# Kernel optimization log

Hardware: AMD Instinct MI355X
Metric: run time of the kernel (lower is better)

The kernel has to match this reference:

```python
import jax, jax.numpy as jnp
import numpy as np

N = 50000      # nodes
E = 1600000    # edges (avg degree 32)
IN, H, OUT, ED = 16, 128, 64, 16


def setup_inputs() -> dict:
    key = jax.random.key(0)
    ks = jax.random.split(key, 24)

    def w(k, shape):
        return jax.random.normal(k, shape, jnp.float32) / np.float32(np.sqrt(shape[0]))

    inp = {
        "x": jax.random.normal(ks[0], (N, IN), jnp.float32),
        "edge_attr": jax.random.normal(ks[1], (E, ED), jnp.float32),
        "edge_src": jax.random.randint(ks[2], (E,), 0, N, jnp.int32),
        "edge_dst": jax.random.randint(ks[3], (E,), 0, N, jnp.int32),
    }
    dims = [(IN, H, H), (H, H, H), (H, H, OUT)]
    i = 4
    for l, (din, dh, dout) in enumerate(dims):
        inp[f"we{l}"] = w(ks[i], (ED, din)); inp[f"be{l}"] = jnp.zeros((din,), jnp.float32)
        inp[f"w1{l}"] = w(ks[i + 1], (din, dh)); inp[f"b1{l}"] = jnp.zeros((dh,), jnp.float32)
        inp[f"w2{l}"] = w(ks[i + 2], (dh, dout)); inp[f"b2{l}"] = jnp.zeros((dout,), jnp.float32)
        i += 3
    inp["rw1"] = w(ks[i], (OUT, H)); inp["rb1"] = jnp.zeros((H,), jnp.float32)
    inp["rw2"] = w(ks[i + 1], (H, IN)); inp["rb2"] = jnp.zeros((IN,), jnp.float32)
    return inp


def reference(x, edge_attr, edge_src, edge_dst,
              we0, be0, w10, b10, w20, b20,
              we1, be1, w11, b11, w21, b21,
              we2, be2, w12, b12, w22, b22,
              rw1, rb1, rw2, rb2):
    layers = [(we0, be0, w10, b10, w20, b20),
              (we1, be1, w11, b11, w21, b21),
              (we2, be2, w12, b12, w22, b22)]
    n = x.shape[0]

    def phi(h):
        # GIN with edge features (GINE): h_i = MLP(h_i + sum_j relu(h_j + W_e e_ij))
        for idx, (we, be, w1, b1, w2, b2) in enumerate(layers):
            e = edge_attr @ we + be                                  # [E, d_in]
            msg = jax.nn.relu(h[edge_src] + e)                       # [E, d_in]
            agg = jax.ops.segment_sum(msg, edge_dst, num_segments=n)  # [N, d_in]
            h = jax.nn.relu((h + agg) @ w1 + b1) @ w2 + b2           # conv MLP
            if idx < len(layers) - 1:
                h = jax.nn.relu(h)
        return h

    out = phi(x) + phi(-x)                       # sign invariance, [N, OUT]
    out = jax.nn.relu(out @ rw1 + rb1) @ rw2 + rb2  # rho readout, [N, IN]
    return out
```

## Files before the change

### kernel.cpp

```cpp
#include <hip/hip_runtime.h>

constexpr int DHID = 128;

typedef __attribute__((ext_vector_type(8))) short bf16x8v;
typedef __attribute__((ext_vector_type(4))) float f32x4v;

__device__ __forceinline__ float b2f(unsigned short u) {
    union { unsigned int i; float f; } v;
    v.i = ((unsigned int)u) << 16;
    return v.f;
}
__device__ __forceinline__ unsigned short f2b(float f) {
    union { float f; unsigned int i; } v;
    v.f = f;
    unsigned int x = v.i;
    return (unsigned short)((x + 0x7fff + ((x >> 16) & 1)) >> 16);
}
__device__ __forceinline__ unsigned int pack2(float a, float b) {
    return (unsigned int)f2b(a) | ((unsigned int)f2b(b) << 16);
}
__device__ __forceinline__ float bres(float w) { return w - b2f(f2b(w)); }
__device__ __forceinline__ void dot2b(float& acc, unsigned int a, unsigned int b) {
    asm("v_dot2_f32_bf16 %0, %1, %2, %0" : "+v"(acc) : "v"(a), "v"(b));
}

__global__ __launch_bounds__(256)
void init_h0(const float* __restrict__ x, float* __restrict__ H0,
             unsigned short* __restrict__ H0B, int n) {
    int i = blockIdx.x * 256 + threadIdx.x;
    if (i < n * 16) {
        int r = i >> 4, c = i & 15;
        float v = x[i];
        H0[(size_t)(2 * r) * 16 + c] = v;
        H0[(size_t)(2 * r + 1) * 16 + c] = -v;
        H0B[(size_t)(2 * r) * 16 + c] = f2b(v);
        H0B[(size_t)(2 * r + 1) * 16 + c] = f2b(-v);
    }
}

__global__ __launch_bounds__(256)
void sum_signs(const float* __restrict__ H3, float* __restrict__ S, int n) {
    int i = blockIdx.x * 256 + threadIdx.x;
    if (i < n * 64) {
        int r = i >> 6;
        S[i] = H3[i + (size_t)r * 64] + H3[i + (size_t)r * 64 + 64];
    }
}

__global__ __launch_bounds__(256)
void csr_count(const int* __restrict__ DST, int* __restrict__ deg, int E_) {
    int e = blockIdx.x * 256 + threadIdx.x;
    if (e < E_) atomicAdd(&deg[DST[e]], 1);
}

__global__ __launch_bounds__(256)
void scan1(const int* __restrict__ deg, int* __restrict__ off,
           int* __restrict__ bsum, int n) {
    __shared__ int s[256];
    int tid = threadIdx.x;
    int i = blockIdx.x * 256 + tid;
    int v = (i < n) ? deg[i] : 0;
    s[tid] = v;
    __syncthreads();
    for (int d = 1; d < 256; d <<= 1) {
        int t = (tid >= d) ? s[tid - d] : 0;
        __syncthreads();
        if (tid >= d) s[tid] += t;
        __syncthreads();
    }
    if (i < n) off[i] = s[tid] - v;
    if (tid == 255) bsum[blockIdx.x] = s[255];
}

__global__ __launch_bounds__(256)
void scan2(int* __restrict__ bsum, int nb) {
    __shared__ int s[256];
    int tid = threadIdx.x;
    int v = (tid < nb) ? bsum[tid] : 0;
    s[tid] = v;
    __syncthreads();
    for (int d = 1; d < 256; d <<= 1) {
        int t = (tid >= d) ? s[tid - d] : 0;
        __syncthreads();
        if (tid >= d) s[tid] += t;
        __syncthreads();
    }
    if (tid < nb) bsum[tid] = s[tid] - v;
}

__global__ __launch_bounds__(256)
void scan3(int* __restrict__ off, int* __restrict__ pos,
           const int* __restrict__ bsum, const int* __restrict__ deg, int n) {
    int i = blockIdx.x * 256 + threadIdx.x;
    if (i < n) {
        int o = off[i] + bsum[blockIdx.x];
        off[i] = o;
        pos[i] = o;
        if (i == n - 1) off[n] = o + deg[i];
    }
}

__global__ __launch_bounds__(256)
void csr_fill(const int* __restrict__ SRC, const int* __restrict__ DST,
              const float* __restrict__ EA, int* __restrict__ pos,
              int* __restrict__ csrsrc, uint4* __restrict__ EABS, int E_) {
    int e = blockIdx.x * 256 + threadIdx.x;
    if (e < E_) {
        int d = DST[e];
        int j = atomicAdd(&pos[d], 1);
        csrsrc[j] = SRC[e];
        const float4* ea4 = (const float4*)(EA + (size_t)e * 16);
        float4 q0 = ea4[0], q1 = ea4[1], q2 = ea4[2], q3 = ea4[3];
        uint4 o0, o1;
        o0.x = pack2(q0.x, q0.y); o0.y = pack2(q0.z, q0.w);
        o0.z = pack2(q1.x, q1.y); o0.w = pack2(q1.z, q1.w);
        o1.x = pack2(q2.x, q2.y); o1.y = pack2(q2.z, q2.w);
        o1.z = pack2(q3.x, q3.y); o1.w = pack2(q3.z, q3.w);
        EABS[(size_t)2 * j] = o0;
        EABS[(size_t)2 * j + 1] = o1;
    }
}

__global__ __launch_bounds__(256)
void agg_gather128(const int* __restrict__ CSRS, const int* __restrict__ OFF,
                   const unsigned short* __restrict__ EABS,
                   const float* __restrict__ WE, const float* __restrict__ BE,
                   const unsigned short* __restrict__ HB,
                   float* __restrict__ AGG, int n) {
    __shared__ float esm_all[4][16][132];
    const int tid = threadIdx.x;
    const int wv = tid >> 6;
    const int lane = tid & 63;
    const int node = blockIdx.x * 4 + wv;
    if (node >= n) return;
    float (*esm)[132] = esm_all[wv];

    const int col = lane & 15;
    const int grp = lane >> 4;
    const int klo = (grp & 1) * 8;

    bf16x8v bfrag[8];
#pragma unroll
    for (int cb = 0; cb < 8; ++cb) {
        bf16x8v b;
#pragma unroll
        for (int i = 0; i < 8; ++i) {
            float w = WE[(klo + i) * 128 + cb * 16 + col];
            unsigned short hi = f2b(w);
            unsigned short lo = f2b(bres(w));
            b[i] = (short)(grp >= 2 ? lo : hi);
        }
        bfrag[cb] = b;
    }
    float bias[8];
#pragma unroll
    for (int cb = 0; cb < 8; ++cb) bias[cb] = BE[cb * 16 + col];

    const int o = lane & 31;
    const int s = o >> 4;
    const int co = (o & 15) * 8;
    const int ep = lane >> 5;

    float acc[8];
#pragma unroll
    for (int i = 0; i < 8; ++i) acc[i] = 0.f;

    const int j0 = OFF[node], j1 = OFF[node + 1];
    const char* ebase = (const char*)EABS;

    for (int base = j0; base < j1; base += 16) {
        const int rem = j1 - base;
        uint4 a4 = *(const uint4*)(ebase + ((size_t)(base + col) << 5) +
                                   ((grp & 1) << 4));
        bf16x8v afrag = __builtin_bit_cast(bf16x8v, a4);
#pragma unroll
        for (int cb = 0; cb < 8; ++cb) {
            f32x4v c = {bias[cb], bias[cb], bias[cb], bias[cb]};
            f32x4v ev = __builtin_amdgcn_mfma_f32_16x16x32_bf16(afrag, bfrag[cb],
                                                                c, 0, 0, 0);
#pragma unroll
            for (int r = 0; r < 4; ++r) {
                const int slot = grp * 4 + r;
                esm[slot][cb * 16 + col] = (slot < rem) ? ev[r] : -1e30f;
            }
        }
        int srcs[8];
#pragma unroll
        for (int i = 0; i < 8; ++i) {
            const int eidx = base + 2 * i + ep;
            srcs[i] = CSRS[eidx < j1 ? eidx : (j1 - 1)];
        }
        uint4 hvv[8];
#pragma unroll
        for (int i = 0; i < 8; ++i)
            hvv[i] = *(const uint4*)(HB + (((size_t)(2 * srcs[i] + s)) << 7) + co);
#pragma unroll
        for (int i = 0; i < 8; ++i) {
            const uint4 hv = hvv[i];
            const float4* ep4 = (const float4*)&esm[2 * i + ep][co];
            float4 e0 = ep4[0], e1 = ep4[1];
            acc[0] += fmaxf(b2f(hv.x & 0xffff) + e0.x, 0.f);
            acc[1] += fmaxf(b2f(hv.x >> 16)    + e0.y, 0.f);
            acc[2] += fmaxf(b2f(hv.y & 0xffff) + e0.z, 0.f);
            acc[3] += fmaxf(b2f(hv.y >> 16)    + e0.w, 0.f);
            acc[4] += fmaxf(b2f(hv.z & 0xffff) + e1.x, 0.f);
            acc[5] += fmaxf(b2f(hv.z >> 16)    + e1.y, 0.f);
            acc[6] += fmaxf(b2f(hv.w & 0xffff) + e1.z, 0.f);
            acc[7] += fmaxf(b2f(hv.w >> 16)    + e1.w, 0.f);
        }
    }
#pragma unroll
    for (int i = 0; i < 8; ++i) acc[i] += __shfl_xor(acc[i], 32);
    if (lane < 32) {
        float* arow = AGG + (size_t)(2 * node + s) * 128 + co;
        float4 v0 = make_float4(acc[0], acc[1], acc[2], acc[3]);
        float4 v1 = make_float4(acc[4], acc[5], acc[6], acc[7]);
        ((float4*)arow)[0] = v0;
        ((float4*)arow)[1] = v1;
    }
}

__global__ __launch_bounds__(256)
void agg_gather16(const int* __restrict__ CSRS, const int* __restrict__ OFF,
                  const uint4* __restrict__ EABS, const float* __restrict__ WE,
                  const float* __restrict__ BE,
                  const unsigned short* __restrict__ HB,
                  float* __restrict__ AGG, int n) {
    const int l = threadIdx.x & 31;
    const int node = blockIdx.x * 8 + (threadIdx.x >> 5);
    if (node >= n) return;
    const int s = l >> 4;
    const int c = l & 15;
    unsigned int wh[8], wl[8];
#pragma unroll
    for (int t = 0; t < 8; ++t) {
        float a0 = WE[(2 * t) * 16 + c], a1 = WE[(2 * t + 1) * 16 + c];
        wh[t] = pack2(a0, a1);
        wl[t] = pack2(bres(a0), bres(a1));
    }
    const float bev = BE[c];
    float acc = 0.f;
    const int j0 = OFF[node], j1 = OFF[node + 1];
#pragma unroll 4
    for (int j = j0; j < j1; ++j) {
        int src = CSRS[j];
        uint4 p = EABS[(size_t)2 * j], q = EABS[(size_t)2 * j + 1];
        float ec = bev;
        dot2b(ec, p.x, wh[0]); dot2b(ec, p.y, wh[1]);
        dot2b(ec, p.z, wh[2]); dot2b(ec, p.w, wh[3]);
        dot2b(ec, q.x, wh[4]); dot2b(ec, q.y, wh[5]);
        dot2b(ec, q.z, wh[6]); dot2b(ec, q.w, wh[7]);
        dot2b(ec, p.x, wl[0]); dot2b(ec, p.y, wl[1]);
        dot2b(ec, p.z, wl[2]); dot2b(ec, p.w, wl[3]);
        dot2b(ec, q.x, wl[4]); dot2b(ec, q.y, wl[5]);
        dot2b(ec, q.z, wl[6]); dot2b(ec, q.w, wl[7]);
        float hv = b2f(HB[(size_t)(2 * src + s) * 16 + c]);
        acc += fmaxf(hv + ec, 0.f);
    }
    AGG[(size_t)(2 * node + s) * 16 + c] = acc;
}

template <int DIN, int DOUT, bool RELU_OUT, bool HAS_AGG, bool WRITE_B>
__global__ __launch_bounds__(256)
void node_mlp(const float* __restrict__ X, const float* __restrict__ AGG,
              const float* __restrict__ W1, const float* __restrict__ B1,
              const float* __restrict__ W2, const float* __restrict__ B2,
              float* __restrict__ OUT, unsigned short* __restrict__ OUTB,
              int rows) {
    __shared__ float sX[32 * DIN];
    __shared__ float sH[32 * DHID];
    const int tid = threadIdx.x;

    for (int row0 = blockIdx.x * 32; row0 < rows; row0 += gridDim.x * 32) {
        __syncthreads();
        constexpr int DIN4 = DIN / 4;
        for (int i = tid; i < 32 * DIN4; i += 256) {
            int r = i / DIN4, k4 = i % DIN4;
            int gr = row0 + r;
            float4 v = make_float4(0.f, 0.f, 0.f, 0.f);
            if (gr < rows) {
                v = ((const float4*)X)[(size_t)gr * DIN4 + k4];
                if (HAS_AGG) {
                    float4 a = ((const float4*)AGG)[(size_t)gr * DIN4 + k4];
                    v.x += a.x; v.y += a.y; v.z += a.z; v.w += a.w;
                }
            }
            ((float4*)sX)[i] = v;
        }
        __syncthreads();
        {
            const int c = tid & 63;
            const int r0 = tid >> 6;
            float acc[8][2];
            const float b1a = B1[c], b1b = B1[c + 64];
#pragma unroll
            for (int j = 0; j < 8; ++j) {
                acc[j][0] = b1a;
                acc[j][1] = b1b;
            }
#pragma unroll 2
            for (int k4 = 0; k4 < DIN / 4; ++k4) {
                const int k = 4 * k4;
                float wa[4], wb[4];
#pragma unroll
                for (int kk = 0; kk < 4; ++kk) {
                    wa[kk] = W1[(k + kk) * DHID + c];
                    wb[kk] = W1[(k + kk) * DHID + c + 64];
                }
#pragma unroll
                for (int j = 0; j < 8; ++j) {
                    float4 xv = ((const float4*)sX)[((r0 + 4 * j) * DIN + k) >> 2];
                    acc[j][0] += xv.x * wa[0]; acc[j][1] += xv.x * wb[0];
                    acc[j][0] += xv.y * wa[1]; acc[j][1] += xv.y * wb[1];
                    acc[j][0] += xv.z * wa[2]; acc[j][1] += xv.z * wb[2];
                    acc[j][0] += xv.w * wa[3]; acc[j][1] += xv.w * wb[3];
                }
            }
#pragma unroll
            for (int j = 0; j < 8; ++j) {
                int r = r0 + 4 * j;
                sH[r * DHID + c] = fmaxf(acc[j][0], 0.f);
                sH[r * DHID + c + 64] = fmaxf(acc[j][1], 0.f);
            }
        }
        __syncthreads();
        {
            constexpr int HALF = DOUT / 2;
            constexpr int RP = 256 / HALF;
            constexpr int ITER = 32 / RP;
            const int c = tid % HALF;
            const int r0 = tid / HALF;
            float acc[ITER][2];
            const float bz0 = B2[c], bz1 = B2[c + HALF];
#pragma unroll
            for (int j = 0; j < ITER; ++j) {
                acc[j][0] = bz0;
                acc[j][1] = bz1;
            }
#pragma unroll 2
            for (int k4 = 0; k4 < DHID / 4; ++k4) {
                const int k = 4 * k4;
                float wa[4], wb[4];
#pragma unroll
                for (int kk = 0; kk < 4; ++kk) {
                    wa[kk] = W2[(k + kk) * DOUT + c];
                    wb[kk] = W2[(k + kk) * DOUT + c + HALF];
                }
#pragma unroll
                for (int j = 0; j < ITER; ++j) {
                    float4 hv = ((const float4*)sH)[((r0 + RP * j) * DHID + k) >> 2];
                    acc[j][0] += hv.x * wa[0]; acc[j][1] += hv.x * wb[0];
                    acc[j][0] += hv.y * wa[1]; acc[j][1] += hv.y * wb[1];
                    acc[j][0] += hv.z * wa[2]; acc[j][1] += hv.z * wb[2];
                    acc[j][0] += hv.w * wa[3]; acc[j][1] += hv.w * wb[3];
                }
            }
#pragma unroll
            for (int j = 0; j < ITER; ++j) {
                int gr = row0 + r0 + RP * j;
                if (gr < rows) {
                    float o0 = acc[j][0], o1 = acc[j][1];
                    if (RELU_OUT) {
                        o0 = fmaxf(o0, 0.f);
                        o1 = fmaxf(o1, 0.f);
                    }
                    OUT[(size_t)gr * DOUT + c] = o0;
                    OUT[(size_t)gr * DOUT + c + HALF] = o1;
                    if (WRITE_B) {
                        OUTB[(size_t)gr * DOUT + c] = f2b(o0);
                        OUTB[(size_t)gr * DOUT + c + HALF] = f2b(o1);
                    }
                }
            }
        }
    }
}

extern "C" void kernel_launch(void* const* d_in, const int* in_sizes, int n_in,
                              void* d_out, int out_size, void* d_ws, size_t ws_size,
                              hipStream_t stream) {
    const float* x = (const float*)d_in[0];
    const float* ea = (const float*)d_in[1];
    const int* esrc = (const int*)d_in[2];
    const int* edst = (const int*)d_in[3];
    const float* we0 = (const float*)d_in[4];
    const float* be0 = (const float*)d_in[5];
    const float* w10 = (const float*)d_in[6];
    const float* b10 = (const float*)d_in[7];
    const float* w20 = (const float*)d_in[8];
    const float* b20 = (const float*)d_in[9];
    const float* we1 = (const float*)d_in[10];
    const float* be1 = (const float*)d_in[11];
    const float* w11 = (const float*)d_in[12];
    const float* b11 = (const float*)d_in[13];
    const float* w21 = (const float*)d_in[14];
    const float* b21 = (const float*)d_in[15];
    const float* we2 = (const float*)d_in[16];
    const float* be2 = (const float*)d_in[17];
    const float* w12 = (const float*)d_in[18];
    const float* b12 = (const float*)d_in[19];
    const float* w22 = (const float*)d_in[20];
    const float* b22 = (const float*)d_in[21];
    const float* rw1 = (const float*)d_in[22];
    const float* rb1 = (const float*)d_in[23];
    const float* rw2 = (const float*)d_in[24];
    const float* rb2 = (const float*)d_in[25];

    const int N = in_sizes[0] / 16;
    const int E = in_sizes[2];
    const int M = 2 * N;

    float* HA = (float*)d_ws;
    float* HB = HA + (size_t)M * 128;
    float* AG = HB + (size_t)M * 128;
    unsigned short* Hb = (unsigned short*)(AG + (size_t)M * 128);
    unsigned short* EABS = Hb + (size_t)M * 128;
    int* deg = (int*)(EABS + (size_t)E * 16);
    int* off = deg + N;
    int* pos = off + N + 1;
    int* bsum = pos + N;
    int* csrsrc = bsum + 256;

    const int ntiles = (M + 31) / 32;
    const int eblocks = (E + 255) / 256;
    const int nblocks = (N + 255) / 256;

    hipMemsetAsync(deg, 0, (size_t)N * sizeof(int), stream);
    csr_count<<<eblocks, 256, 0, stream>>>(edst, deg, E);
    scan1<<<nblocks, 256, 0, stream>>>(deg, off, bsum, N);
    scan2<<<1, 256, 0, stream>>>(bsum, nblocks);
    scan3<<<nblocks, 256, 0, stream>>>(off, pos, bsum, deg, N);
    csr_fill<<<eblocks, 256, 0, stream>>>(esrc, edst, ea, pos, csrsrc,
                                          (uint4*)EABS, E);

    init_h0<<<(N * 16 + 255) / 256, 256, 0, stream>>>(x, HA, Hb, N);

    agg_gather16<<<(N + 7) / 8, 256, 0, stream>>>(csrsrc, off, (const uint4*)EABS,
                                                  we0, be0, Hb, AG, N);
    node_mlp<16, 128, true, true, true><<<ntiles, 256, 0, stream>>>(
        HA, AG, w10, b10, w20, b20, HB, Hb, M);

    agg_gather128<<<(N + 3) / 4, 256, 0, stream>>>(csrsrc, off, EABS,
                                                   we1, be1, Hb, AG, N);
    node_mlp<128, 128, true, true, true><<<ntiles, 256, 0, stream>>>(
        HB, AG, w11, b11, w21, b21, HA, Hb, M);

    agg_gather128<<<(N + 3) / 4, 256, 0, stream>>>(csrsrc, off, EABS,
                                                   we2, be2, Hb, AG, N);
    node_mlp<128, 64, false, true, false><<<ntiles, 256, 0, stream>>>(
        HA, AG, w12, b12, w22, b22, HB, nullptr, M);

    sum_signs<<<(N * 64 + 255) / 256, 256, 0, stream>>>(HB, AG, N);
    node_mlp<64, 16, false, false, false><<<(N + 31) / 32, 256, 0, stream>>>(
        AG, nullptr, rw1, rb1, rw2, rb2, (float*)d_out, nullptr, N);
}
```

Measured before the change: 955.0 us.

## Split 128-wide node MLPs into two MFMA kernels with split-bf16 precision

Replaces the fp32 shared-memory node_mlp for the 128-input layers with two MFMA-based kernels. The first computes relu((h+agg)@W1+b1) and writes the hidden activations as hi/lo bf16 pairs. The second computes the W2 projection from those pairs, keeping W2 fragments in registers. Three bf16 MFMA products (hi*hi, lo*hi, hi*lo) approximate fp32 accuracy while using matrix cores instead of scalar FMAs. The trade-off is an extra kernel launch and a round-trip of the hidden activations through global memory, plus a small loss of precision.

Result: slower. 1.086 ms (+13.7%).

```diff
diff --git a/kernel.cpp b/kernel.cpp
--- a/kernel.cpp
+++ b/kernel.cpp
@@ -258,6 +258,184 @@
         acc += fmaxf(hv + ec, 0.f);
     }
     AGG[(size_t)(2 * node + s) * 16 + c] = acc;
+}
+
+__global__ __launch_bounds__(256)
+void mlp_a(const float* __restrict__ X, const float* __restrict__ AGG,
+           const float* __restrict__ W1, const float* __restrict__ B1,
+           unsigned short* __restrict__ Hhi, unsigned short* __restrict__ Hlo,
+           int rows) {
+    __shared__ unsigned short sHi[16][136];
+    __shared__ unsigned short sLo[16][136];
+    const int tid = threadIdx.x;
+    const int w = tid >> 6;
+    const int lane = tid & 63;
+    const int col = lane & 15;
+    const int grp = lane >> 4;
+    const int klo8 = (grp & 1) * 8;
+    const bool hi_lane = grp < 2;
+    const int row0 = blockIdx.x * 128;
+
+    bf16x8v b1f[2][8];
+    float bias1[2];
+#pragma unroll
+    for (int cb = 0; cb < 2; ++cb) {
+        const int cbg = 2 * w + cb;
+#pragma unroll
+        for (int kc = 0; kc < 8; ++kc) {
+            bf16x8v b;
+#pragma unroll
+            for (int i = 0; i < 8; ++i) {
+                float wv = W1[(size_t)(kc * 16 + klo8 + i) * 128 + cbg * 16 + col];
+                b[i] = (short)(hi_lane ? f2b(wv) : f2b(bres(wv)));
+            }
+            b1f[cb][kc] = b;
+        }
+        bias1[cb] = B1[cbg * 16 + col];
+    }
+
+    for (int rg = 0; rg < 8; ++rg) {
+        __syncthreads();
+        {
+            const int r = tid >> 4;
+            const int kb = (tid & 15) * 8;
+            const int gr = row0 + rg * 16 + r;
+            float v[8];
+            if (gr < rows) {
+                const float4* xp = (const float4*)(X + (size_t)gr * 128 + kb);
+                const float4* ap = (const float4*)(AGG + (size_t)gr * 128 + kb);
+                float4 x0 = xp[0], x1 = xp[1], g0 = ap[0], g1 = ap[1];
+                v[0] = x0.x + g0.x; v[1] = x0.y + g0.y;
+                v[2] = x0.z + g0.z; v[3] = x0.w + g0.w;
+                v[4] = x1.x + g1.x; v[5] = x1.y + g1.y;
+                v[6] = x1.z + g1.z; v[7] = x1.w + g1.w;
+            } else {
+#pragma unroll
+                for (int i = 0; i < 8; ++i) v[i] = 0.f;
+            }
+            uint4 ph, pl;
+            ph.x = pack2(v[0], v[1]); ph.y = pack2(v[2], v[3]);
+            ph.z = pack2(v[4], v[5]); ph.w = pack2(v[6], v[7]);
+            pl.x = pack2(bres(v[0]), bres(v[1])); pl.y = pack2(bres(v[2]), bres(v[3]));
+            pl.z = pack2(bres(v[4]), bres(v[5])); pl.w = pack2(bres(v[6]), bres(v[7]));
+            *(uint4*)&sHi[r][kb] = ph;
+            *(uint4*)&sLo[r][kb] = pl;
+        }
+        __syncthreads();
+        f32x4v acc0 = {bias1[0], bias1[0], bias1[0], bias1[0]};
+        f32x4v acc1 = {bias1[1], bias1[1], bias1[1], bias1[1]};
+#pragma unroll
+        for (int kc = 0; kc < 8; ++kc) {
+            bf16x8v a1 = *(const bf16x8v*)&sHi[col][kc * 16 + klo8];
+            bf16x8v a2;
+            if (hi_lane) {
+                a2 = *(const bf16x8v*)&sLo[col][kc * 16 + klo8];
+            } else {
+#pragma unroll
+                for (int i = 0; i < 8; ++i) a2[i] = 0;
+            }
+            acc0 = __builtin_amdgcn_mfma_f32_16x16x32_bf16(a1, b1f[0][kc], acc0, 0, 0, 0);
+            acc0 = __builtin_amdgcn_mfma_f32_16x16x32_bf16(a2, b1f[0][kc], acc0, 0, 0, 0);
+            acc1 = __builtin_amdgcn_mfma_f32_16x16x32_bf16(a1, b1f[1][kc], acc1, 0, 0, 0);
+            acc1 = __builtin_amdgcn_mfma_f32_16x16x32_bf16(a2, b1f[1][kc], acc1, 0, 0, 0);
+        }
+#pragma unroll
+        for (int cb = 0; cb < 2; ++cb) {
+            const f32x4v acc = cb ? acc1 : acc0;
+            const int cbg = 2 * w + cb;
+#pragma unroll
+            for (int r = 0; r < 4; ++r) {
+                const int gr = row0 + rg * 16 + grp * 4 + r;
+                if (gr < rows) {
+                    float vv = fmaxf(acc[r], 0.f);
+                    unsigned short h = f2b(vv);
+                    Hhi[(size_t)gr * 128 + cbg * 16 + col] = h;
+                    Hlo[(size_t)gr * 128 + cbg * 16 + col] = f2b(bres(vv));
+                }
+            }
+        }
+    }
+}
+
+template <int DOUT, bool RELU_OUT, bool WRITE_B>
+__global__ __launch_bounds__(256)
+void mlp_b(const unsigned short* __restrict__ Hhi,
+           const unsigned short* __restrict__ Hlo,
+           const float* __restrict__ W2, const float* __restrict__ B2,
+           float* __restrict__ OUT, unsigned short* __restrict__ OUTB, int rows) {
+    constexpr int NB = DOUT / 16;
+    constexpr int CBW = NB / 4;
+    const int tid = threadIdx.x;
+    const int w = tid >> 6;
+    const int lane = tid & 63;
+    const int col = lane & 15;
+    const int grp = lane >> 4;
+    const int klo8 = (grp & 1) * 8;
+    const bool hi_lane = grp < 2;
+    const int row0 = blockIdx.x * 128;
+
+    bf16x8v b2f0[8], b2f1[8];
+    float bias2[2];
+#pragma unroll
+    for (int cb = 0; cb < CBW; ++cb) {
+        const int cbg = w * CBW + cb;
+#pragma unroll
+        for (int kc = 0; kc < 8; ++kc) {
+            bf16x8v b;
+#pragma unroll
+            for (int i = 0; i < 8; ++i) {
+                float wv = W2[(size_t)(kc * 16 + klo8 + i) * DOUT + cbg * 16 + col];
+                b[i] = (short)(hi_lane ? f2b(wv) : f2b(bres(wv)));
+            }
+            if (cb == 0) b2f0[kc] = b; else b2f1[kc] = b;
+        }
+        bias2[cb] = B2[cbg * 16 + col];
+    }
+
+    for (int rg = 0; rg < 8; ++rg) {
+        int arow = row0 + rg * 16 + col;
+        if (arow >= rows) arow = rows - 1;
+        const unsigned short* hp = Hhi + (size_t)arow * 128;
+        const unsigned short* lp = Hlo + (size_t)arow * 128;
+        bf16x8v a1[8], a2[8];
+#pragma unroll
+        for (int kc = 0; kc < 8; ++kc) {
+            a1[kc] = *(const bf16x8v*)(hp + kc * 16 + klo8);
+            if (hi_lane) {
+                a2[kc] = *(const bf16x8v*)(lp + kc * 16 + klo8);
+            } else {
+#pragma unroll
+                for (int i = 0; i < 8; ++i) a2[kc][i] = 0;
+            }
+        }
+        f32x4v acc0 = {bias2[0], bias2[0], bias2[0], bias2[0]};
+        f32x4v acc1 = {bias2[1], bias2[1], bias2[1], bias2[1]};
+#pragma unroll
+        for (int kc = 0; kc < 8; ++kc) {
+            acc0 = __builtin_amdgcn_mfma_f32_16x16x32_bf16(a1[kc], b2f0[kc], acc0, 0, 0, 0);
+            acc0 = __builtin_amdgcn_mfma_f32_16x16x32_bf16(a2[kc], b2f0[kc], acc0, 0, 0, 0);
+            if (CBW == 2) {
+                acc1 = __builtin_amdgcn_mfma_f32_16x16x32_bf16(a1[kc], b2f1[kc], acc1, 0, 0, 0);
+                acc1 = __builtin_amdgcn_mfma_f32_16x16x32_bf16(a2[kc], b2f1[kc], acc1, 0, 0, 0);
+            }
+        }
+#pragma unroll
+        for (int cb = 0; cb < CBW; ++cb) {
+            const f32x4v acc = cb ? acc1 : acc0;
+            const int cbg = w * CBW + cb;
+#pragma unroll
+            for (int r = 0; r < 4; ++r) {
+                const int gr = row0 + rg * 16 + grp * 4 + r;
+                if (gr < rows) {
+                    float o = acc[r];
+                    if (RELU_OUT) o = fmaxf(o, 0.f);
+                    OUT[(size_t)gr * DOUT + cbg * 16 + col] = o;
+                    if (WRITE_B)
+                        OUTB[(size_t)gr * DOUT + cbg * 16 + col] = f2b(o);
+                }
+            }
+        }
+    }
 }
 
 template <int DIN, int DOUT, bool RELU_OUT, bool HAS_AGG, bool WRITE_B>
@@ -414,7 +592,9 @@
     float* HB = HA + (size_t)M * 128;
     float* AG = HB + (size_t)M * 128;
     unsigned short* Hb = (unsigned short*)(AG + (size_t)M * 128);
-    unsigned short* EABS = Hb + (size_t)M * 128;
+    unsigned short* Hhi = Hb + (size_t)M * 128;
+    unsigned short* Hlo = Hhi + (size_t)M * 128;
+    unsigned short* EABS = Hlo + (size_t)M * 128;
     int* deg = (int*)(EABS + (size_t)E * 16);
     int* off = deg + N;
     int* pos = off + N + 1;
@@ -424,6 +604,7 @@
     const int ntiles = (M + 31) / 32;
     const int eblocks = (E + 255) / 256;
     const int nblocks = (N + 255) / 256;
+    const int mtiles = (M + 127) / 128;
 
     hipMemsetAsync(deg, 0, (size_t)N * sizeof(int), stream);
     csr_count<<<eblocks, 256, 0, stream>>>(edst, deg, E);
@@ -442,13 +623,15 @@
 
     agg_gather128<<<(N + 3) / 4, 256, 0, stream>>>(csrsrc, off, EABS,
                                                    we1, be1, Hb, AG, N);
-    node_mlp<128, 128, true, true, true><<<ntiles, 256, 0, stream>>>(
-        HB, AG, w11, b11, w21, b21, HA, Hb, M);
+    mlp_a<<<mtiles, 256, 0, stream>>>(HB, AG, w11, b11, Hhi, Hlo, M);
+    mlp_b<128, true, true><<<mtiles, 256, 0, stream>>>(Hhi, Hlo, w21, b21,
+                                                       HA, Hb, M);
 
     agg_gather128<<<(N + 3) / 4, 256, 0, stream>>>(csrsrc, off, EABS,
                                                    we2, be2, Hb, AG, N);
-    node_mlp<128, 64, false, true, false><<<ntiles, 256, 0, stream>>>(
-        HA, AG, w12, b12, w22, b22, HB, nullptr, M);
+    mlp_a<<<mtiles, 256, 0, stream>>>(HA, AG, w12, b12, Hhi, Hlo, M);
+    mlp_b<64, false, false><<<mtiles, 256, 0, stream>>>(Hhi, Hlo, w22, b22,
+                                                        HB, nullptr, M);
 
     sum_signs<<<(N * 64 + 255) / 256, 256, 0, stream>>>(HB, AG, N);
     node_mlp<64, 16, false, false, false><<<(N + 31) / 32, 256, 0, stream>>>(
```
